# Performance work log

Hardware: AMD Instinct MI355X
Metric: run time of the kernel (lower is better)

The kernel has to match this reference:

```python
import jax, jax.numpy as jnp
import numpy as np


def setup_inputs() -> dict:
    key = jax.random.key(0)
    ks = jax.random.split(key, 10)
    N, E = 50000, 1600000
    IN, H, OUT = 32, 64, 16
    x = jax.random.normal(ks[0], (N, IN), dtype=jnp.float32)
    edge_index = jax.random.randint(ks[1], (2, E), 0, N, dtype=jnp.int64)
    edge_attr = jax.random.normal(ks[2], (E, 3), dtype=jnp.float32)
    s1 = 1.0 / np.sqrt(2 * IN + 3)
    W1 = jax.random.uniform(ks[3], (2 * IN + 3, H), jnp.float32, -s1, s1)
    b1 = jax.random.uniform(ks[4], (H,), jnp.float32, -s1, s1)
    s2 = 1.0 / np.sqrt(H)
    W2 = jax.random.uniform(ks[5], (H, H), jnp.float32, -s2, s2)
    b2 = jax.random.uniform(ks[6], (H,), jnp.float32, -s2, s2)
    Wo = jax.random.uniform(ks[7], (H, OUT), jnp.float32, -s2, s2)
    bo = jax.random.uniform(ks[8], (OUT,), jnp.float32, -s2, s2)
    return {"x": x, "edge_index": edge_index, "edge_attr": edge_attr,
            "W1": W1, "b1": b1, "W2": W2, "b2": b2, "Wo": Wo, "bo": bo}


def reference(x, edge_index, edge_attr, W1, b1, W2, b2, Wo, bo):
    N = x.shape[0]
    src, dst = edge_index[0], edge_index[1]  # PyG: x_j = x[src], x_i = x[dst]
    x_i = x[dst]                      # [E, IN]
    x_j = x[src]                      # [E, IN]
    tmp = jnp.concatenate([x_i, x_j - x_i, edge_attr], axis=1)  # [E, 2*IN+3]
    h = jax.nn.relu(tmp @ W1 + b1)    # [E, H]
    msg = h @ W2 + b2                 # [E, H]
    # max-aggregate messages to destination nodes; empty segments -> 0 (PyG fill)
    agg = jax.ops.segment_max(msg, dst, num_segments=N)
    agg = jnp.where(jnp.isfinite(agg), agg, 0.0)
    out = jax.nn.sigmoid(agg @ Wo + bo)  # [N, OUT]
    return out
```

## Files before the change

kernel.cpp:

```cpp
#include <hip/hip_runtime.h>

#define IN_F 32
#define HID 64
#define OUTF 16
#define DPB 128
#define CAPB 5120
#define RSL 80
#define EPB 4096
#define OVF_CAP 65536
#define ORD_NEG_INF 0x007FFFFFu

typedef _Float16 v8h __attribute__((ext_vector_type(8)));
typedef float v4f __attribute__((ext_vector_type(4)));

__device__ __forceinline__ unsigned ordenc(float v) {
  unsigned b = __float_as_uint(v);
  return (b & 0x80000000u) ? ~b : (b | 0x80000000u);
}
__device__ __forceinline__ float orddec(unsigned u) {
  unsigned b = (u & 0x80000000u) ? (u & 0x7FFFFFFFu) : ~u;
  return __uint_as_float(b);
}
__device__ __forceinline__ unsigned short f2h_bits(float f) {
  _Float16 h = (_Float16)f; unsigned short u; __builtin_memcpy(&u, &h, 2); return u;
}
__device__ __forceinline__ float h_bits2f(unsigned short u) {
  _Float16 h; __builtin_memcpy(&h, &u, 2); return (float)h;
}

__global__ __launch_bounds__(256) void p0_kernel(
    const int* __restrict__ ei,
    const float* __restrict__ x, const float* __restrict__ W1,
    const float* __restrict__ b1,
    float* __restrict__ P, _Float16* __restrict__ Q,
    unsigned* __restrict__ hist, int E, int N, int nSB, int NBKT)
{
  if (blockIdx.x < (unsigned)nSB) {
    __shared__ unsigned h[512];
    for (int i = threadIdx.x; i < NBKT; i += 256) h[i] = 0;
    __syncthreads();
    const int base = blockIdx.x * EPB;
#pragma unroll 1
    for (int r = 0; r < 4; ++r) {
      const int b2 = base + r * 1024;
      int dd[4]; bool vv[4];
#pragma unroll
      for (int i = 0; i < 4; ++i) {
        int e = b2 + i * 256 + threadIdx.x;
        vv[i] = e < E;
        dd[i] = ei[(size_t)E + (vv[i] ? e : 0)];
      }
#pragma unroll
      for (int i = 0; i < 4; ++i)
        if (vv[i]) atomicAdd(&h[dd[i] >> 7], 1u);
    }
    __syncthreads();
    for (int i = threadIdx.x; i < NBKT; i += 256)
      hist[(size_t)blockIdx.x * NBKT + i] = h[i];
    return;
  }
  const int lane = threadIdx.x & 63;
  float w1d[IN_F], w1b[IN_F];
#pragma unroll
  for (int c = 0; c < IN_F; ++c) {
    w1b[c] = W1[(IN_F + c) * HID + lane];
    w1d[c] = W1[c * HID + lane] - w1b[c];
  }
  const float b1v = b1[lane];
  int gw = __builtin_amdgcn_readfirstlane((((int)blockIdx.x - nSB) << 2) | (threadIdx.x >> 6));
  const int nwaves = 512 << 2;
  for (int n = gw; n < N; n += nwaves) {
    float p = b1v, q = 0.f;
#pragma unroll
    for (int c = 0; c < IN_F; ++c) {
      float xv = x[n * IN_F + c];
      p = fmaf(xv, w1d[c], p);
      q = fmaf(xv, w1b[c], q);
    }
    P[n * HID + lane] = p;
    Q[n * HID + lane] = (_Float16)q;
  }
}

__global__ __launch_bounds__(256) void scan_kernel(
    unsigned* __restrict__ hist, unsigned* __restrict__ totals,
    int nblk, int NBKT)
{
  __shared__ unsigned s[256];
  const int b = blockIdx.x;
  const int tid = threadIdx.x;
  unsigned running = 0;
  const int nch = (nblk + 255) >> 8;
  for (int c = 0; c < nch; ++c) {
    const int idx = c * 256 + tid;
    unsigned v = (idx < nblk) ? hist[(size_t)idx * NBKT + b] : 0u;
    s[tid] = v;
    __syncthreads();
#pragma unroll
    for (int off = 1; off < 256; off <<= 1) {
      unsigned t = (tid >= off) ? s[tid - off] : 0u;
      __syncthreads();
      s[tid] += t;
      __syncthreads();
    }
    const unsigned incl = s[tid];
    const unsigned tot = s[255];
    if (idx < nblk) hist[(size_t)idx * NBKT + b] = running + (incl - v);
    running += tot;
    __syncthreads();
  }
  if (tid == 0) totals[b] = running;
}

__global__ __launch_bounds__(256) void p1_kernel(
    const int* __restrict__ ei, const float* __restrict__ ea,
    const unsigned* __restrict__ hist,
    uint2* __restrict__ cu, unsigned char* __restrict__ cdlo,
    uint4* __restrict__ ovf, int* __restrict__ ovf_cnt,
    int E, int NBKT)
{
  __shared__ unsigned h2[512];
  for (int i = threadIdx.x; i < NBKT; i += 256) h2[i] = 0;
  __syncthreads();
  const int base = blockIdx.x * EPB;
#pragma unroll 1
  for (int r = 0; r < 4; ++r) {
    const int b2 = base + r * 1024;
    int s[4], d[4]; bool v[4];
#pragma unroll
    for (int i = 0; i < 4; ++i) {
      int e = b2 + i * 256 + threadIdx.x;
      v[i] = e < E;
      int ec = v[i] ? e : 0;
      s[i] = ei[ec];
      d[i] = ei[(size_t)E + ec];
    }
    float a0[4], a1[4], a2[4];
#pragma unroll
    for (int i = 0; i < 4; ++i) {
      int ec = v[i] ? (b2 + i * 256 + threadIdx.x) : 0;
      a0[i] = ea[ec * 3 + 0]; a1[i] = ea[ec * 3 + 1]; a2[i] = ea[ec * 3 + 2];
    }
#pragma unroll
    for (int i = 0; i < 4; ++i) {
      if (!v[i]) continue;
      const int b = d[i] >> 7;
      const unsigned rr = atomicAdd(&h2[b], 1u);
      const unsigned pos = hist[(size_t)blockIdx.x * NBKT + b] + rr;
      uint2 pay;
      pay.x = (unsigned)s[i] | ((unsigned)f2h_bits(a0[i]) << 16);
      pay.y = (unsigned)f2h_bits(a1[i]) | ((unsigned)f2h_bits(a2[i]) << 16);
      if (pos < CAPB) {
        cu[(size_t)b * CAPB + pos] = pay;
        cdlo[(size_t)b * CAPB + pos] = (unsigned char)(d[i] & (DPB - 1));
      } else {
        int oi = atomicAdd(ovf_cnt, 1);
        if (oi < OVF_CAP) ovf[oi] = make_uint4(pay.x, pay.y, (unsigned)d[i], 0u);
      }
    }
  }
}

__global__ __launch_bounds__(512) void p2_kernel(
    const uint2* __restrict__ cu, const unsigned char* __restrict__ cdlo,
    const unsigned* __restrict__ totals,
    uint2* __restrict__ rec, int* __restrict__ cnt,
    uint4* __restrict__ ovf, int* __restrict__ ovf_cnt, int N)
{
  __shared__ int c[DPB];
  const int b = blockIdx.x;
  const int tid = threadIdx.x;
  if (tid < DPB) c[tid] = 0;
  __syncthreads();
  const int nE = (int)min(totals[b], (unsigned)CAPB);
  for (int i = tid; i < nE; i += 512) {
    const uint2 pay = cu[(size_t)b * CAPB + i];
    const int dlo = cdlo[(size_t)b * CAPB + i];
    const int r = atomicAdd(&c[dlo], 1);
    const int d = b * DPB + dlo;
    if (r < RSL) rec[(size_t)d * RSL + r] = pay;
    else {
      int oi = atomicAdd(ovf_cnt, 1);
      if (oi < OVF_CAP) ovf[oi] = make_uint4(pay.x, pay.y, (unsigned)d, 0u);
    }
  }
  __syncthreads();
  if (tid < DPB) {
    const int d = b * DPB + tid;
    if (d < N) cnt[d] = c[tid];
  }
}

__global__ __launch_bounds__(256) void bucket_kernel(
    const uint2* __restrict__ rec, const int* __restrict__ cnt,
    const float* __restrict__ W1, const float* __restrict__ W2,
    const float* __restrict__ P, const _Float16* __restrict__ Q,
    unsigned* __restrict__ agg, int N)
{
  __shared__ __align__(16) _Float16 hB[4][16][72];

  const int wave = threadIdx.x >> 6;
  const int lane = threadIdx.x & 63;
  const int quad = lane >> 4;
  const int eidx = lane & 15;
  const int mych = ((eidx >> 2) << 4) + (quad << 2) + (eidx & 3);

  v8h a_frag[4][2];
#pragma unroll
  for (int t = 0; t < 4; ++t)
#pragma unroll
    for (int ks = 0; ks < 2; ++ks)
#pragma unroll
      for (int j = 0; j < 8; ++j)
        a_frag[t][ks][j] = (_Float16)W2[(ks * 32 + quad * 8 + j) * HID + t * 16 + eidx];

  const float w1c0 = W1[(2 * IN_F + 0) * HID + lane];
  const float w1c1 = W1[(2 * IN_F + 1) * HID + lane];
  const float w1c2 = W1[(2 * IN_F + 2) * HID + lane];

  const int gwave = __builtin_amdgcn_readfirstlane((blockIdx.x << 2) | wave);
  const int nw = gridDim.x << 2;

  int d = gwave;
  if (d >= N) return;

  int m; uint2 r0, r1; float pP;
  auto prefetch = [&](int dd) {
    m = min(cnt[dd], RSL);
    if (lane < m) r0 = rec[(size_t)dd * RSL + lane];
    if (m > 64) {
      if (64 + lane < m) r1 = rec[(size_t)dd * RSL + 64 + lane];
    }
    pP = P[(size_t)dd * HID + lane];
  };

  prefetch(d);

  while (d < N) {
    const int dn = d + nw;
    const int m_cur = m;
    const float pvl = pP;
    uint2 ra = r0, rb = r1;

    if (m_cur > 0) {
      {
        const int lm = m_cur - 1;
        unsigned rlx, rly;
        if (lm < 64) {
          rlx = (unsigned)__builtin_amdgcn_readlane((int)ra.x, lm);
          rly = (unsigned)__builtin_amdgcn_readlane((int)ra.y, lm);
        } else {
          rlx = (unsigned)__builtin_amdgcn_readlane((int)rb.x, lm & 63);
          rly = (unsigned)__builtin_amdgcn_readlane((int)rb.y, lm & 63);
        }
        if (lane >= m_cur)      { ra.x = rlx; ra.y = rly; }
        if (lane + 64 >= m_cur) { rb.x = rlx; rb.y = rly; }
      }

      float qvA[8], qvB[8];
#pragma unroll
      for (int i = 0; i < 8; ++i) {
        unsigned sx = (unsigned)__builtin_amdgcn_readlane((int)ra.x, i) & 0xFFFFu;
        qvA[i] = (float)Q[(size_t)sx * HID + lane];
      }
#pragma unroll
      for (int i = 0; i < 8; ++i) {
        unsigned sx = (unsigned)__builtin_amdgcn_readlane((int)ra.x, 8 + i) & 0xFFFFu;
        qvB[i] = (float)Q[(size_t)sx * HID + lane];
      }

      if (dn < N) prefetch(dn);

      float maxv[4][4];
#pragma unroll
      for (int t = 0; t < 4; ++t)
#pragma unroll
        for (int r = 0; r < 4; ++r) maxv[t][r] = -INFINITY;

      const int ntile = (m_cur + 15) >> 4;
      const int noct = ntile << 1;
      for (int tb = 0; tb < ntile; ++tb) {
        const unsigned rsx = (tb < 4) ? ra.x : rb.x;
        const unsigned rsy = (tb < 4) ? ra.y : rb.y;
        const int b16 = (tb & 3) << 4;

#pragma unroll
        for (int i = 0; i < 8; ++i) {
          const unsigned rx = (unsigned)__builtin_amdgcn_readlane((int)rsx, b16 + i);
          const unsigned ry = (unsigned)__builtin_amdgcn_readlane((int)rsy, b16 + i);
          float pre = pvl + qvA[i];
          pre = fmaf(h_bits2f((unsigned short)(rx >> 16)), w1c0, pre);
          pre = fmaf(h_bits2f((unsigned short)(ry & 0xFFFFu)), w1c1, pre);
          pre = fmaf(h_bits2f((unsigned short)(ry >> 16)), w1c2, pre);
          hB[wave][i][lane] = (_Float16)fmaxf(pre, 0.f);
        }
        {
          const int o = 2 * tb + 2;
          if (o < noct) {
            const unsigned rox = (o < 8) ? ra.x : rb.x;
            const int bo = (o & 7) << 3;
#pragma unroll
            for (int i = 0; i < 8; ++i) {
              unsigned sx = (unsigned)__builtin_amdgcn_readlane((int)rox, bo + i) & 0xFFFFu;
              qvA[i] = (float)Q[(size_t)sx * HID + lane];
            }
          }
        }
#pragma unroll
        for (int i = 0; i < 8; ++i) {
          const unsigned rx = (unsigned)__builtin_amdgcn_readlane((int)rsx, b16 + 8 + i);
          const unsigned ry = (unsigned)__builtin_amdgcn_readlane((int)rsy, b16 + 8 + i);
          float pre = pvl + qvB[i];
          pre = fmaf(h_bits2f((unsigned short)(rx >> 16)), w1c0, pre);
          pre = fmaf(h_bits2f((unsigned short)(ry & 0xFFFFu)), w1c1, pre);
          pre = fmaf(h_bits2f((unsigned short)(ry >> 16)), w1c2, pre);
          hB[wave][8 + i][lane] = (_Float16)fmaxf(pre, 0.f);
        }
        {
          const int o = 2 * tb + 3;
          if (o < noct) {
            const unsigned rox = (o < 8) ? ra.x : rb.x;
            const int bo = (o & 7) << 3;
#pragma unroll
            for (int i = 0; i < 8; ++i) {
              unsigned sx = (unsigned)__builtin_amdgcn_readlane((int)rox, bo + i) & 0xFFFFu;
              qvB[i] = (float)Q[(size_t)sx * HID + lane];
            }
          }
        }
        __builtin_amdgcn_wave_barrier();

        const v8h bf0 = *(const v8h*)&hB[wave][eidx][quad * 8];
        const v8h bf1 = *(const v8h*)&hB[wave][eidx][32 + quad * 8];
#pragma unroll
        for (int t = 0; t < 4; ++t) {
          v4f acc = (v4f){0.f, 0.f, 0.f, 0.f};
          acc = __builtin_amdgcn_mfma_f32_16x16x32_f16(a_frag[t][0], bf0, acc, 0, 0, 0);
          acc = __builtin_amdgcn_mfma_f32_16x16x32_f16(a_frag[t][1], bf1, acc, 0, 0, 0);
#pragma unroll
          for (int r = 0; r < 4; ++r) maxv[t][r] = fmaxf(maxv[t][r], acc[r]);
        }
        __builtin_amdgcn_wave_barrier();
      }

#pragma unroll
      for (int t = 0; t < 4; ++t)
#pragma unroll
        for (int r = 0; r < 4; ++r) {
          float v = maxv[t][r];
          v = fmaxf(v, __shfl_xor(v, 1, 64));
          v = fmaxf(v, __shfl_xor(v, 2, 64));
          v = fmaxf(v, __shfl_xor(v, 4, 64));
          v = fmaxf(v, __shfl_xor(v, 8, 64));
          maxv[t][r] = v;
        }
      float val = maxv[0][0];
#pragma unroll
      for (int t = 0; t < 4; ++t)
#pragma unroll
        for (int r = 0; r < 4; ++r)
          val = (eidx == t * 4 + r) ? maxv[t][r] : val;
      agg[(size_t)d * HID + mych] = ordenc(val);
    } else {
      if (dn < N) prefetch(dn);
      agg[(size_t)d * HID + lane] = ORD_NEG_INF;
    }
    d = dn;
  }
}

__global__ __launch_bounds__(256) void overflow_kernel(
    const uint4* __restrict__ ovf, const int* __restrict__ ovf_cnt,
    const float* __restrict__ W1, const float* __restrict__ W2,
    const float* __restrict__ P, const _Float16* __restrict__ Q,
    unsigned* __restrict__ agg)
{
  __shared__ float hsh[4][HID];
  const int wave = threadIdx.x >> 6;
  const int lane = threadIdx.x & 63;

  int M = *ovf_cnt;
  if (M > OVF_CAP) M = OVF_CAP;
  if (M == 0) return;

  float w2r[HID];
#pragma unroll
  for (int j = 0; j < HID; ++j) w2r[j] = W2[j * HID + lane];
  const float w1c0 = W1[(2 * IN_F + 0) * HID + lane];
  const float w1c1 = W1[(2 * IN_F + 1) * HID + lane];
  const float w1c2 = W1[(2 * IN_F + 2) * HID + lane];

  const int gwave = __builtin_amdgcn_readfirstlane((blockIdx.x << 2) | wave);
  const int nw = gridDim.x << 2;
  for (int k = gwave; k < M; k += nw) {
    const uint4 o = ovf[k];
    const int s = (int)(o.x & 0xFFFFu);
    const int d = (int)o.z;
    float pre = P[(size_t)d * HID + lane] + (float)Q[(size_t)s * HID + lane];
    pre = fmaf(h_bits2f((unsigned short)(o.x >> 16)), w1c0, pre);
    pre = fmaf(h_bits2f((unsigned short)(o.y & 0xFFFFu)), w1c1, pre);
    pre = fmaf(h_bits2f((unsigned short)(o.y >> 16)), w1c2, pre);
    hsh[wave][lane] = fmaxf(pre, 0.f);
    __builtin_amdgcn_wave_barrier();
    float mv = 0.f;
#pragma unroll
    for (int j = 0; j < HID; ++j) mv = fmaf(hsh[wave][j], w2r[j], mv);
    atomicMax(&agg[(size_t)d * HID + lane], ordenc(mv));
    __builtin_amdgcn_wave_barrier();
  }
}

__global__ __launch_bounds__(256) void out_kernel(
    const unsigned* __restrict__ agg,
    const float* __restrict__ b2,
    const float* __restrict__ Wo, const float* __restrict__ bo,
    float* __restrict__ out, int N)
{
  __shared__ float Wos[HID * OUTF];
  __shared__ float bos[OUTF];
  __shared__ float b2s[HID];
  __shared__ float aggs[16][HID + 1];

  for (int i = threadIdx.x; i < HID * OUTF; i += 256) Wos[i] = Wo[i];
  if (threadIdx.x < OUTF) bos[threadIdx.x] = bo[threadIdx.x];
  if (threadIdx.x < HID) b2s[threadIdx.x] = b2[threadIdx.x];
  __syncthreads();

  const int nodeBase = blockIdx.x * 16;
  {
    int ln = threadIdx.x >> 4;
    int k0 = (threadIdx.x & 15) * 4;
    int n = nodeBase + ln;
    if (n < N) {
      const uint4 u = *(const uint4*)&agg[(size_t)n * HID + k0];
      aggs[ln][k0 + 0] = (u.x == ORD_NEG_INF) ? 0.f : orddec(u.x) + b2s[k0 + 0];
      aggs[ln][k0 + 1] = (u.y == ORD_NEG_INF) ? 0.f : orddec(u.y) + b2s[k0 + 1];
      aggs[ln][k0 + 2] = (u.z == ORD_NEG_INF) ? 0.f : orddec(u.z) + b2s[k0 + 2];
      aggs[ln][k0 + 3] = (u.w == ORD_NEG_INF) ? 0.f : orddec(u.w) + b2s[k0 + 3];
    }
  }
  __syncthreads();
  {
    int ln = threadIdx.x >> 4;
    int o = threadIdx.x & 15;
    int n = nodeBase + ln;
    if (n < N) {
      float acc = bos[o];
#pragma unroll
      for (int k = 0; k < HID; ++k) acc = fmaf(aggs[ln][k], Wos[k * OUTF + o], acc);
      out[n * OUTF + o] = 1.f / (1.f + __expf(-acc));
    }
  }
}

extern "C" void kernel_launch(void* const* d_in, const int* in_sizes, int n_in,
                              void* d_out, int out_size, void* d_ws, size_t ws_size,
                              hipStream_t stream) {
  const float* x  = (const float*)d_in[0];
  const int*   ei = (const int*)d_in[1];
  const float* ea = (const float*)d_in[2];
  const float* W1 = (const float*)d_in[3];
  const float* b1 = (const float*)d_in[4];
  const float* W2 = (const float*)d_in[5];
  const float* b2 = (const float*)d_in[6];
  const float* Wo = (const float*)d_in[7];
  const float* bo = (const float*)d_in[8];
  float* out = (float*)d_out;

  const int N = in_sizes[0] / IN_F;
  const int E = in_sizes[1] / 2;
  const int NBKT = (N + DPB - 1) / DPB;
  const int nSB  = (E + EPB - 1) / EPB;

  char* w = (char*)d_ws;
  auto align16 = [](size_t v) { return (v + 15) & ~(size_t)15; };
  float*     Pp   = (float*)w;       w += align16((size_t)N * HID * 4);
  _Float16*  Qp   = (_Float16*)w;    w += align16((size_t)N * HID * 2);
  unsigned*  agg  = (unsigned*)w;    w += align16((size_t)N * HID * 4);
  uint2*     rec  = (uint2*)w;       w += align16((size_t)N * RSL * 8);
  uint2*     cu   = (uint2*)w;       w += align16((size_t)NBKT * CAPB * 8);
  unsigned*  hist = (unsigned*)w;    w += align16((size_t)nSB * NBKT * 4);
  unsigned*  tot  = (unsigned*)w;    w += align16((size_t)NBKT * 4);
  int*       cnt  = (int*)w;         w += align16((size_t)N * 4);
  unsigned char* cdlo = (unsigned char*)w; w += align16((size_t)NBKT * CAPB);
  int*   ovf_cnt  = (int*)w;         w += 16;
  uint4*     ovf  = (uint4*)w;

  hipMemsetAsync(ovf_cnt, 0, 16, stream);

  p0_kernel<<<nSB + 512, 256, 0, stream>>>(ei, x, W1, b1, Pp, Qp, hist, E, N, nSB, NBKT);
  scan_kernel<<<NBKT, 256, 0, stream>>>(hist, tot, nSB, NBKT);
  p1_kernel<<<nSB, 256, 0, stream>>>(ei, ea, hist, cu, cdlo, ovf, ovf_cnt, E, NBKT);
  p2_kernel<<<NBKT, 512, 0, stream>>>(cu, cdlo, tot, rec, cnt, ovf, ovf_cnt, N);
  bucket_kernel<<<4096, 256, 0, stream>>>(rec, cnt, W1, W2, Pp, Qp, agg, N);
  overflow_kernel<<<256, 256, 0, stream>>>(ovf, ovf_cnt, W1, W2, Pp, Qp, agg);
  out_kernel<<<(N + 15) / 16, 256, 0, stream>>>(agg, b2, Wo, bo, out, N);
}
```

Baseline: 258.3 us.

## Replace histogram scan with per-block atomic bucket allocation fused into scatter

Removes the separate scan kernel and the second scatter kernel. Each edge block now counts its destination buckets in shared memory, reserves a range in each bucket with one global atomicAdd per bucket, and scatters its edges in the same kernel. This cuts two launches and the global histogram traffic in exchange for global atomics and a non-deterministic order of edges within each bucket, which max-aggregation tolerates.

After: 253.4 us. About the same (-1.9%).

```diff
diff --git a/kernel.cpp b/kernel.cpp
--- a/kernel.cpp
+++ b/kernel.cpp
@@ -28,16 +28,20 @@
   _Float16 h; __builtin_memcpy(&h, &u, 2); return (float)h;
 }
 
-__global__ __launch_bounds__(256) void p0_kernel(
-    const int* __restrict__ ei,
+__global__ __launch_bounds__(256) void p1_kernel(
+    const int* __restrict__ ei, const float* __restrict__ ea,
     const float* __restrict__ x, const float* __restrict__ W1,
     const float* __restrict__ b1,
     float* __restrict__ P, _Float16* __restrict__ Q,
-    unsigned* __restrict__ hist, int E, int N, int nSB, int NBKT)
+    unsigned* __restrict__ bktAlloc,
+    uint2* __restrict__ cu, unsigned char* __restrict__ cdlo,
+    uint4* __restrict__ ovf, int* __restrict__ ovf_cnt,
+    int E, int N, int nSB, int NBKT)
 {
   if (blockIdx.x < (unsigned)nSB) {
-    __shared__ unsigned h[512];
-    for (int i = threadIdx.x; i < NBKT; i += 256) h[i] = 0;
+    __shared__ unsigned hcnt[512];
+    __shared__ unsigned hbase[512];
+    for (int i = threadIdx.x; i < NBKT; i += 256) hcnt[i] = 0;
     __syncthreads();
     const int base = blockIdx.x * EPB;
 #pragma unroll 1
@@ -52,11 +56,51 @@
       }
 #pragma unroll
       for (int i = 0; i < 4; ++i)
-        if (vv[i]) atomicAdd(&h[dd[i] >> 7], 1u);
+        if (vv[i]) atomicAdd(&hcnt[dd[i] >> 7], 1u);
     }
     __syncthreads();
-    for (int i = threadIdx.x; i < NBKT; i += 256)
-      hist[(size_t)blockIdx.x * NBKT + i] = h[i];
+    for (int i = threadIdx.x; i < NBKT; i += 256) {
+      const unsigned c = hcnt[i];
+      hbase[i] = c ? atomicAdd(&bktAlloc[i], c) : 0u;
+      hcnt[i] = 0;
+    }
+    __syncthreads();
+#pragma unroll 1
+    for (int r = 0; r < 4; ++r) {
+      const int b2 = base + r * 1024;
+      int s[4], d[4]; bool v[4];
+#pragma unroll
+      for (int i = 0; i < 4; ++i) {
+        int e = b2 + i * 256 + threadIdx.x;
+        v[i] = e < E;
+        int ec = v[i] ? e : 0;
+        s[i] = ei[ec];
+        d[i] = ei[(size_t)E + ec];
+      }
+      float a0[4], a1[4], a2[4];
+#pragma unroll
+      for (int i = 0; i < 4; ++i) {
+        int ec = v[i] ? (b2 + i * 256 + threadIdx.x) : 0;
+        a0[i] = ea[ec * 3 + 0]; a1[i] = ea[ec * 3 + 1]; a2[i] = ea[ec * 3 + 2];
+      }
+#pragma unroll
+      for (int i = 0; i < 4; ++i) {
+        if (!v[i]) continue;
+        const int b = d[i] >> 7;
+        const unsigned rr = atomicAdd(&hcnt[b], 1u);
+        const unsigned pos = hbase[b] + rr;
+        uint2 pay;
+        pay.x = (unsigned)s[i] | ((unsigned)f2h_bits(a0[i]) << 16);
+        pay.y = (unsigned)f2h_bits(a1[i]) | ((unsigned)f2h_bits(a2[i]) << 16);
+        if (pos < CAPB) {
+          cu[(size_t)b * CAPB + pos] = pay;
+          cdlo[(size_t)b * CAPB + pos] = (unsigned char)(d[i] & (DPB - 1));
+        } else {
+          int oi = atomicAdd(ovf_cnt, 1);
+          if (oi < OVF_CAP) ovf[oi] = make_uint4(pay.x, pay.y, (unsigned)d[i], 0u);
+        }
+      }
+    }
     return;
   }
   const int lane = threadIdx.x & 63;
@@ -82,88 +126,9 @@
   }
 }
 
-__global__ __launch_bounds__(256) void scan_kernel(
-    unsigned* __restrict__ hist, unsigned* __restrict__ totals,
-    int nblk, int NBKT)
-{
-  __shared__ unsigned s[256];
-  const int b = blockIdx.x;
-  const int tid = threadIdx.x;
-  unsigned running = 0;
-  const int nch = (nblk + 255) >> 8;
-  for (int c = 0; c < nch; ++c) {
-    const int idx = c * 256 + tid;
-    unsigned v = (idx < nblk) ? hist[(size_t)idx * NBKT + b] : 0u;
-    s[tid] = v;
-    __syncthreads();
-#pragma unroll
-    for (int off = 1; off < 256; off <<= 1) {
-      unsigned t = (tid >= off) ? s[tid - off] : 0u;
-      __syncthreads();
-      s[tid] += t;
-      __syncthreads();
-    }
-    const unsigned incl = s[tid];
-    const unsigned tot = s[255];
-    if (idx < nblk) hist[(size_t)idx * NBKT + b] = running + (incl - v);
-    running += tot;
-    __syncthreads();
-  }
-  if (tid == 0) totals[b] = running;
-}
-
-__global__ __launch_bounds__(256) void p1_kernel(
-    const int* __restrict__ ei, const float* __restrict__ ea,
-    const unsigned* __restrict__ hist,
-    uint2* __restrict__ cu, unsigned char* __restrict__ cdlo,
-    uint4* __restrict__ ovf, int* __restrict__ ovf_cnt,
-    int E, int NBKT)
-{
-  __shared__ unsigned h2[512];
-  for (int i = threadIdx.x; i < NBKT; i += 256) h2[i] = 0;
-  __syncthreads();
-  const int base = blockIdx.x * EPB;
-#pragma unroll 1
-  for (int r = 0; r < 4; ++r) {
-    const int b2 = base + r * 1024;
-    int s[4], d[4]; bool v[4];
-#pragma unroll
-    for (int i = 0; i < 4; ++i) {
-      int e = b2 + i * 256 + threadIdx.x;
-      v[i] = e < E;
-      int ec = v[i] ? e : 0;
-      s[i] = ei[ec];
-      d[i] = ei[(size_t)E + ec];
-    }
-    float a0[4], a1[4], a2[4];
-#pragma unroll
-    for (int i = 0; i < 4; ++i) {
-      int ec = v[i] ? (b2 + i * 256 + threadIdx.x) : 0;
-      a0[i] = ea[ec * 3 + 0]; a1[i] = ea[ec * 3 + 1]; a2[i] = ea[ec * 3 + 2];
-    }
-#pragma unroll
-    for (int i = 0; i < 4; ++i) {
-      if (!v[i]) continue;
-      const int b = d[i] >> 7;
-      const unsigned rr = atomicAdd(&h2[b], 1u);
-      const unsigned pos = hist[(size_t)blockIdx.x * NBKT + b] + rr;
-      uint2 pay;
-      pay.x = (unsigned)s[i] | ((unsigned)f2h_bits(a0[i]) << 16);
-      pay.y = (unsigned)f2h_bits(a1[i]) | ((unsigned)f2h_bits(a2[i]) << 16);
-      if (pos < CAPB) {
-        cu[(size_t)b * CAPB + pos] = pay;
-        cdlo[(size_t)b * CAPB + pos] = (unsigned char)(d[i] & (DPB - 1));
-      } else {
-        int oi = atomicAdd(ovf_cnt, 1);
-        if (oi < OVF_CAP) ovf[oi] = make_uint4(pay.x, pay.y, (unsigned)d[i], 0u);
-      }
-    }
-  }
-}
-
 __global__ __launch_bounds__(512) void p2_kernel(
     const uint2* __restrict__ cu, const unsigned char* __restrict__ cdlo,
-    const unsigned* __restrict__ totals,
+    const unsigned* __restrict__ bktAlloc,
     uint2* __restrict__ rec, int* __restrict__ cnt,
     uint4* __restrict__ ovf, int* __restrict__ ovf_cnt, int N)
 {
@@ -172,7 +137,7 @@
   const int tid = threadIdx.x;
   if (tid < DPB) c[tid] = 0;
   __syncthreads();
-  const int nE = (int)min(totals[b], (unsigned)CAPB);
+  const int nE = (int)min(bktAlloc[b], (unsigned)CAPB);
   for (int i = tid; i < nE; i += 512) {
     const uint2 pay = cu[(size_t)b * CAPB + i];
     const int dlo = cdlo[(size_t)b * CAPB + i];
@@ -479,19 +444,17 @@
   unsigned*  agg  = (unsigned*)w;    w += align16((size_t)N * HID * 4);
   uint2*     rec  = (uint2*)w;       w += align16((size_t)N * RSL * 8);
   uint2*     cu   = (uint2*)w;       w += align16((size_t)NBKT * CAPB * 8);
-  unsigned*  hist = (unsigned*)w;    w += align16((size_t)nSB * NBKT * 4);
-  unsigned*  tot  = (unsigned*)w;    w += align16((size_t)NBKT * 4);
   int*       cnt  = (int*)w;         w += align16((size_t)N * 4);
   unsigned char* cdlo = (unsigned char*)w; w += align16((size_t)NBKT * CAPB);
+  unsigned* bktAlloc = (unsigned*)w; w += align16((size_t)NBKT * 4);
   int*   ovf_cnt  = (int*)w;         w += 16;
   uint4*     ovf  = (uint4*)w;
 
-  hipMemsetAsync(ovf_cnt, 0, 16, stream);
-
-  p0_kernel<<<nSB + 512, 256, 0, stream>>>(ei, x, W1, b1, Pp, Qp, hist, E, N, nSB, NBKT);
-  scan_kernel<<<NBKT, 256, 0, stream>>>(hist, tot, nSB, NBKT);
-  p1_kernel<<<nSB, 256, 0, stream>>>(ei, ea, hist, cu, cdlo, ovf, ovf_cnt, E, NBKT);
-  p2_kernel<<<NBKT, 512, 0, stream>>>(cu, cdlo, tot, rec, cnt, ovf, ovf_cnt, N);
+  hipMemsetAsync(bktAlloc, 0, align16((size_t)NBKT * 4) + 16, stream);
+
+  p1_kernel<<<nSB + 512, 256, 0, stream>>>(
+      ei, ea, x, W1, b1, Pp, Qp, bktAlloc, cu, cdlo, ovf, ovf_cnt, E, N, nSB, NBKT);
+  p2_kernel<<<NBKT, 512, 0, stream>>>(cu, cdlo, bktAlloc, rec, cnt, ovf, ovf_cnt, N);
   bucket_kernel<<<4096, 256, 0, stream>>>(rec, cnt, W1, W2, Pp, Qp, agg, N);
   overflow_kernel<<<256, 256, 0, stream>>>(ovf, ovf_cnt, W1, W2, Pp, Qp, agg);
   out_kernel<<<(N + 15) / 16, 256, 0, stream>>>(agg, b2, Wo, bo, out, N);
```
